# Performance work log

Measured on AMD Instinct MI355X. Metric: run time of the kernel, lower is better.

Reference implementation:

```python
import jax, jax.numpy as jnp
import numpy as np

B, C, H, W = 4, 64, 128, 128
HEADS, DIM_HEAD = 8, 64
INNER = HEADS * DIM_HEAD
EPS = 1e-12  # torch F.normalize default eps


def setup_inputs() -> dict:
    key = jax.random.key(0)
    ks = jax.random.split(key, 6)
    s_in = 1.0 / np.sqrt(C)
    s_pr = 1.0 / np.sqrt(INNER)
    return {
        "x_in": jax.random.normal(ks[0], (B, C, H, W), dtype=jnp.float32),
        "Wq": jax.random.uniform(ks[1], (C, INNER), jnp.float32, -s_in, s_in),
        "Wk": jax.random.uniform(ks[2], (C, INNER), jnp.float32, -s_in, s_in),
        "Wv": jax.random.uniform(ks[3], (C, INNER), jnp.float32, -s_in, s_in),
        "Wp": jax.random.uniform(ks[4], (INNER, C), jnp.float32, -s_pr, s_pr),
        "bp": jax.random.uniform(ks[5], (C,), jnp.float32, -s_pr, s_pr),
        "rescale": jnp.ones((HEADS, 1, 1), dtype=jnp.float32),
    }


def _l2norm(t):
    # normalize along last axis (the token axis n), matching F.normalize(p=2)
    n = jnp.sqrt(jnp.sum(t * t, axis=-1, keepdims=True))
    return t / jnp.maximum(n, EPS)


def reference(x_in, Wq, Wk, Wv, Wp, bp, rescale):
    b, c, h, w = x_in.shape
    n = h * w
    x = x_in.transpose(0, 2, 3, 1).reshape(b, n, c)  # [b, n, c]

    def heads_first(t):  # [b, n, inner] -> [b, heads, d, n]
        return t.reshape(b, n, HEADS, DIM_HEAD).transpose(0, 2, 3, 1)

    q = _l2norm(heads_first(x @ Wq))  # [b, H, d, n]
    k = _l2norm(heads_first(x @ Wk))
    v = heads_first(x @ Wv)

    # channel-channel attention: attn[d, e] = sum_n k[d, n] * q[e, n]
    attn = jnp.einsum('bhdn,bhen->bhde', k, q) * rescale  # [b, H, d, d]
    attn = jax.nn.softmax(attn, axis=-1)

    o = jnp.einsum('bhde,bhen->bhdn', attn, v)            # [b, H, d, n]
    o = o.transpose(0, 3, 1, 2).reshape(b, n, INNER)      # [b, n, inner]
    out = (o @ Wp + bp).reshape(b, h, w, c).transpose(0, 3, 1, 2)  # [b, c, h, w]
    return out, attn
```

## Files before the change

kernel.cpp:

```cpp
#include <hip/hip_runtime.h>
#include <math.h>

#define BB 4
#define CC 64
#define NN 16384
#define HEADS 8
#define INNER 512

__global__ __launch_bounds__(256) void k_gram(const float* __restrict__ x,
                                              float* __restrict__ part,
                                              int nslice) {
    const int s = blockIdx.x, b = blockIdx.y;
    const int t = threadIdx.x;
    const int g = t >> 6;
    const int lane = t & 63;
    const int ti = lane >> 3, tj = lane & 7;
    __shared__ float xs[64][65];
    float acc[8][8];
#pragma unroll
    for (int i = 0; i < 8; i++)
#pragma unroll
        for (int j = 0; j < 8; j++) acc[i][j] = 0.f;

    const float* xb = x + (size_t)b * CC * NN;
    const int cols = NN / nslice;
    const int ntiles = cols >> 6;
    const int nbase = s * cols;
    for (int tile = 0; tile < ntiles; ++tile) {
        const int n0 = nbase + tile * 64;
#pragma unroll
        for (int k = 0; k < 4; k++) {
            int f = k * 256 + t;
            int c = f >> 4, j4 = f & 15;
            const float4 v = *reinterpret_cast<const float4*>(xb + (size_t)c * NN + n0 + j4 * 4);
            xs[c][j4 * 4 + 0] = v.x; xs[c][j4 * 4 + 1] = v.y;
            xs[c][j4 * 4 + 2] = v.z; xs[c][j4 * 4 + 3] = v.w;
        }
        __syncthreads();
#pragma unroll
        for (int nn = 0; nn < 16; ++nn) {
            const int n = g * 16 + nn;
            float a[8], bv[8];
#pragma unroll
            for (int i = 0; i < 8; i++) a[i] = xs[ti * 8 + i][n];
#pragma unroll
            for (int j = 0; j < 8; j++) bv[j] = xs[tj * 8 + j][n];
#pragma unroll
            for (int i = 0; i < 8; i++)
#pragma unroll
                for (int j = 0; j < 8; j++)
                    acc[i][j] = fmaf(a[i], bv[j], acc[i][j]);
        }
        __syncthreads();
    }
    for (int gg = 0; gg < 4; ++gg) {
        if (g == gg) {
#pragma unroll
            for (int i = 0; i < 8; i++)
#pragma unroll
                for (int j = 0; j < 8; j++) {
                    if (gg == 0) xs[ti * 8 + i][tj * 8 + j] = acc[i][j];
                    else         xs[ti * 8 + i][tj * 8 + j] += acc[i][j];
                }
        }
        __syncthreads();
    }
    float* p = part + (size_t)(b * nslice + s) * 4096;
#pragma unroll
    for (int k = 0; k < 16; k++) {
        int f = k * 256 + t;
        p[f] = xs[f >> 6][f & 63];
    }
}

__global__ __launch_bounds__(256) void k_redG(const float* __restrict__ part,
                                              float* __restrict__ G,
                                              int nslice) {
    const int b = blockIdx.y;
    const int idx = blockIdx.x * 256 + threadIdx.x;
    const float* p = part + (size_t)b * nslice * 4096 + idx;
    float s0 = 0.f, s1 = 0.f, s2 = 0.f, s3 = 0.f;
    for (int s = 0; s < nslice; s += 4) {
        s0 += p[(size_t)s * 4096];
        s1 += p[(size_t)(s + 1) * 4096];
        s2 += p[(size_t)(s + 2) * 4096];
        s3 += p[(size_t)(s + 3) * 4096];
    }
    G[(size_t)b * 4096 + idx] = (s0 + s1) + (s2 + s3);
}

__global__ __launch_bounds__(256) void k_attn(const float* __restrict__ G,
                                              const float* __restrict__ Wq,
                                              const float* __restrict__ Wk,
                                              const float* __restrict__ Wv,
                                              const float* __restrict__ rescale,
                                              float* __restrict__ attn_out,
                                              float* __restrict__ wveff) {
    const int bh = blockIdx.x;
    const int b = bh >> 3, h = bh & 7;
    const int t = threadIdx.x;
    const int ti = t >> 4, tj = t & 15;
    __shared__ float Gs[64][65], Ws[64][65], Ts[64][65];
    __shared__ float qn[64], kn[64];

    for (int k = 0; k < 16; k++) { int f = k * 256 + t; Gs[f >> 6][f & 63] = G[(size_t)b * 4096 + f]; }
    for (int k = 0; k < 16; k++) { int f = k * 256 + t; int c = f >> 6, e = f & 63;
        Ws[c][e] = Wq[(size_t)c * INNER + h * 64 + e]; }
    __syncthreads();

    {
        float acc[4][4] = {};
        for (int c2 = 0; c2 < 64; c2++) {
            float a[4], bv[4];
#pragma unroll
            for (int i = 0; i < 4; i++) a[i] = Gs[ti * 4 + i][c2];
#pragma unroll
            for (int j = 0; j < 4; j++) bv[j] = Ws[c2][tj * 4 + j];
#pragma unroll
            for (int i = 0; i < 4; i++)
#pragma unroll
                for (int j = 0; j < 4; j++) acc[i][j] = fmaf(a[i], bv[j], acc[i][j]);
        }
#pragma unroll
        for (int i = 0; i < 4; i++)
#pragma unroll
            for (int j = 0; j < 4; j++) Ts[ti * 4 + i][tj * 4 + j] = acc[i][j];
    }
    __syncthreads();
    if (t < 64) {
        float s = 0.f;
        for (int c = 0; c < 64; c++) s += Ws[c][t] * Ts[c][t];
        qn[t] = fmaxf(sqrtf(s), 1e-12f);
    }
    __syncthreads();
    for (int k = 0; k < 16; k++) { int f = k * 256 + t; int c = f >> 6, e = f & 63;
        Ws[c][e] = Wk[(size_t)c * INNER + h * 64 + e]; }
    __syncthreads();

    float S[4][4] = {};
    for (int c = 0; c < 64; c++) {
        float a[4], bv[4];
#pragma unroll
        for (int i = 0; i < 4; i++) a[i] = Ws[c][ti * 4 + i];
#pragma unroll
        for (int j = 0; j < 4; j++) bv[j] = Ts[c][tj * 4 + j];
#pragma unroll
        for (int i = 0; i < 4; i++)
#pragma unroll
            for (int j = 0; j < 4; j++) S[i][j] = fmaf(a[i], bv[j], S[i][j]);
    }
    __syncthreads();

    {
        float acc[4][4] = {};
        for (int c2 = 0; c2 < 64; c2++) {
            float a[4], bv[4];
#pragma unroll
            for (int i = 0; i < 4; i++) a[i] = Gs[ti * 4 + i][c2];
#pragma unroll
            for (int j = 0; j < 4; j++) bv[j] = Ws[c2][tj * 4 + j];
#pragma unroll
            for (int i = 0; i < 4; i++)
#pragma unroll
                for (int j = 0; j < 4; j++) acc[i][j] = fmaf(a[i], bv[j], acc[i][j]);
        }
        __syncthreads();
#pragma unroll
        for (int i = 0; i < 4; i++)
#pragma unroll
            for (int j = 0; j < 4; j++) Ts[ti * 4 + i][tj * 4 + j] = acc[i][j];
    }
    __syncthreads();
    if (t < 64) {
        float s = 0.f;
        for (int c = 0; c < 64; c++) s += Ws[c][t] * Ts[c][t];
        kn[t] = fmaxf(sqrtf(s), 1e-12f);
    }
    __syncthreads();

    const float resc = rescale[h];
    float qinv[4];
#pragma unroll
    for (int j = 0; j < 4; j++) qinv[j] = 1.f / qn[tj * 4 + j];
    float p[4][4];
#pragma unroll
    for (int i = 0; i < 4; i++) {
        const float ki = resc / kn[ti * 4 + i];
        float m = -3.402823466e+38f;
#pragma unroll
        for (int j = 0; j < 4; j++) {
            float L = S[i][j] * ki * qinv[j];
            p[i][j] = L;
            m = fmaxf(m, L);
        }
        for (int o = 1; o < 16; o <<= 1) m = fmaxf(m, __shfl_xor(m, o, 64));
        float ssum = 0.f;
#pragma unroll
        for (int j = 0; j < 4; j++) { p[i][j] = expf(p[i][j] - m); ssum += p[i][j]; }
        for (int o = 1; o < 16; o <<= 1) ssum += __shfl_xor(ssum, o, 64);
        const float inv = 1.f / ssum;
#pragma unroll
        for (int j = 0; j < 4; j++) p[i][j] *= inv;
    }

    float* ao = attn_out + (size_t)bh * 64 * 64;
#pragma unroll
    for (int i = 0; i < 4; i++) {
        float4 v; v.x = p[i][0]; v.y = p[i][1]; v.z = p[i][2]; v.w = p[i][3];
        *reinterpret_cast<float4*>(ao + (size_t)(ti * 4 + i) * 64 + tj * 4) = v;
#pragma unroll
        for (int j = 0; j < 4; j++) Gs[ti * 4 + i][tj * 4 + j] = p[i][j];
    }
    __syncthreads();
    for (int k = 0; k < 16; k++) { int f = k * 256 + t; int c = f >> 6, e = f & 63;
        Ws[c][e] = Wv[(size_t)c * INNER + h * 64 + e]; }
    __syncthreads();

    {
        float acc[4][4] = {};
        for (int e = 0; e < 64; e++) {
            float a[4], bv[4];
#pragma unroll
            for (int i = 0; i < 4; i++) a[i] = Ws[ti * 4 + i][e];
#pragma unroll
            for (int j = 0; j < 4; j++) bv[j] = Gs[tj * 4 + j][e];
#pragma unroll
            for (int i = 0; i < 4; i++)
#pragma unroll
                for (int j = 0; j < 4; j++) acc[i][j] = fmaf(a[i], bv[j], acc[i][j]);
        }
        float* wvp = wveff + (size_t)b * CC * INNER;
#pragma unroll
        for (int i = 0; i < 4; i++) {
            float4 v; v.x = acc[i][0]; v.y = acc[i][1]; v.z = acc[i][2]; v.w = acc[i][3];
            *reinterpret_cast<float4*>(wvp + (size_t)(ti * 4 + i) * INNER + h * 64 + tj * 4) = v;
        }
    }
}

__global__ __launch_bounds__(256) void k_mpart(const float* __restrict__ wveff,
                                               const float* __restrict__ Wp,
                                               float* __restrict__ mpart) {
    const int cg = blockIdx.x, b = blockIdx.y;
    const int t = threadIdx.x, ti = t >> 4, tj = t & 15;
    __shared__ float Vs[64][65], Ps[64][65];
    float acc[4][4] = {};
    for (int sub = 0; sub < 2; ++sub) {
        const int hd0 = cg * 128 + sub * 64;
#pragma unroll
        for (int k = 0; k < 4; k++) {
            int f = k * 256 + t; int c = f >> 4, k4 = f & 15;
            float4 v = *reinterpret_cast<const float4*>(wveff + (size_t)b * CC * INNER + (size_t)c * INNER + hd0 + k4 * 4);
            Vs[c][k4 * 4 + 0] = v.x; Vs[c][k4 * 4 + 1] = v.y; Vs[c][k4 * 4 + 2] = v.z; Vs[c][k4 * 4 + 3] = v.w;
            float4 w = *reinterpret_cast<const float4*>(Wp + (size_t)(hd0 + c) * 64 + k4 * 4);
            Ps[c][k4 * 4 + 0] = w.x; Ps[c][k4 * 4 + 1] = w.y; Ps[c][k4 * 4 + 2] = w.z; Ps[c][k4 * 4 + 3] = w.w;
        }
        __syncthreads();
        for (int k = 0; k < 64; k++) {
            float a[4], bv[4];
#pragma unroll
            for (int i = 0; i < 4; i++) a[i] = Vs[ti * 4 + i][k];
#pragma unroll
            for (int j = 0; j < 4; j++) bv[j] = Ps[k][tj * 4 + j];
#pragma unroll
            for (int i = 0; i < 4; i++)
#pragma unroll
                for (int j = 0; j < 4; j++) acc[i][j] = fmaf(a[i], bv[j], acc[i][j]);
        }
        __syncthreads();
    }
    float* mp = mpart + (size_t)(b * 4 + cg) * 4096;
#pragma unroll
    for (int i = 0; i < 4; i++)
#pragma unroll
        for (int j = 0; j < 4; j++) mp[(ti * 4 + i) * 64 + tj * 4 + j] = acc[i][j];
}

__global__ __launch_bounds__(256) void k_out(const float* __restrict__ x,
                                             const float* __restrict__ mpart,
                                             const float* __restrict__ bp,
                                             float* __restrict__ out) {
    const int sn = blockIdx.x, b = blockIdx.y;
    const int t = threadIdx.x, ti = t >> 4, tj = t & 15;
    __shared__ float Ms[64][65], xs[64][65];
    const float* mp = mpart + (size_t)b * 4 * 4096;
#pragma unroll
    for (int k = 0; k < 16; k++) {
        int f = k * 256 + t;
        float s = mp[f] + mp[4096 + f] + mp[2 * 4096 + f] + mp[3 * 4096 + f];
        Ms[f >> 6][f & 63] = s;
    }
    const int n0 = sn * 64;
    const float* xb = x + (size_t)b * CC * NN;
#pragma unroll
    for (int k = 0; k < 4; k++) {
        int f = k * 256 + t; int c = f >> 4, j4 = f & 15;
        float4 v = *reinterpret_cast<const float4*>(xb + (size_t)c * NN + n0 + j4 * 4);
        xs[c][j4 * 4 + 0] = v.x; xs[c][j4 * 4 + 1] = v.y;
        xs[c][j4 * 4 + 2] = v.z; xs[c][j4 * 4 + 3] = v.w;
    }
    __syncthreads();
    float acc[4][4];
#pragma unroll
    for (int i = 0; i < 4; i++) {
        const float bv = bp[ti * 4 + i];
#pragma unroll
        for (int j = 0; j < 4; j++) acc[i][j] = bv;
    }
    for (int c = 0; c < 64; c++) {
        float m[4], xv[4];
#pragma unroll
        for (int i = 0; i < 4; i++) m[i] = Ms[c][ti * 4 + i];
#pragma unroll
        for (int j = 0; j < 4; j++) xv[j] = xs[c][tj * 4 + j];
#pragma unroll
        for (int i = 0; i < 4; i++)
#pragma unroll
            for (int j = 0; j < 4; j++) acc[i][j] = fmaf(m[i], xv[j], acc[i][j]);
    }
    float* ob = out + (size_t)b * CC * NN;
#pragma unroll
    for (int i = 0; i < 4; i++) {
        float4 v; v.x = acc[i][0]; v.y = acc[i][1]; v.z = acc[i][2]; v.w = acc[i][3];
        *reinterpret_cast<float4*>(ob + (size_t)(ti * 4 + i) * NN + n0 + tj * 4) = v;
    }
}

extern "C" void kernel_launch(void* const* d_in, const int* in_sizes, int n_in,
                              void* d_out, int out_size, void* d_ws, size_t ws_size,
                              hipStream_t stream) {
    const float* x  = (const float*)d_in[0];
    const float* Wq = (const float*)d_in[1];
    const float* Wk = (const float*)d_in[2];
    const float* Wv = (const float*)d_in[3];
    const float* Wp = (const float*)d_in[4];
    const float* bp = (const float*)d_in[5];
    const float* rescale = (const float*)d_in[6];
    float* out = (float*)d_out;
    float* attn_out = out + (size_t)BB * CC * NN;
    float* ws = (float*)d_ws;

    const size_t fixed_floats = (size_t)BB * 4096
                              + (size_t)BB * CC * INNER
                              + (size_t)BB * 4 * 4096;
    int nslice = 64;
    while (nslice > 4 &&
           ((size_t)BB * nslice * 4096 + fixed_floats) * sizeof(float) > ws_size)
        nslice >>= 1;

    float* part  = ws;
    float* G     = part + (size_t)BB * nslice * 4096;
    float* wveff = G + (size_t)BB * 4096;
    float* mpart = wveff + (size_t)BB * CC * INNER;

    hipLaunchKernelGGL(k_gram,  dim3(nslice, BB), dim3(256), 0, stream, x, part, nslice);
    hipLaunchKernelGGL(k_redG,  dim3(16, BB),     dim3(256), 0, stream, part, G, nslice);
    hipLaunchKernelGGL(k_attn,  dim3(BB * HEADS), dim3(256), 0, stream, G, Wq, Wk, Wv, rescale, attn_out, wveff);
    hipLaunchKernelGGL(k_mpart, dim3(4, BB),      dim3(256), 0, stream, wveff, Wp, mpart);
    hipLaunchKernelGGL(k_out,   dim3(NN / 64, BB), dim3(256), 0, stream, x, mpart, bp, out);
}
```

Measured before the change: 140.5 us.

## Fuse Wp projection into attention kernel with atomics and retile Gram kernel

Restructures the Gram kernel so each thread owns a 4x4 tile over the full 64-column tile with transposed float4 LDS reads, which removes the cross-wavegroup shared-memory reduction. The grid grows to 256 slices. The V-effective and Wp products are folded into k_attn, which atomically accumulates per-head contributions into a zeroed M buffer; this drops the k_mpart kernel and the wveff round trip through memory. Several kernels move to float4 LDS loads with padding of 68. In exchange it adds a memset, float atomics with nondeterministic summation order, and a larger partial buffer for k_redG to reduce.

```diff
diff --git a/kernel.cpp b/kernel.cpp
--- a/kernel.cpp
+++ b/kernel.cpp
@@ -12,15 +12,16 @@
                                               int nslice) {
     const int s = blockIdx.x, b = blockIdx.y;
     const int t = threadIdx.x;
-    const int g = t >> 6;
-    const int lane = t & 63;
-    const int ti = lane >> 3, tj = lane & 7;
-    __shared__ float xs[64][65];
-    float acc[8][8];
-#pragma unroll
-    for (int i = 0; i < 8; i++)
-#pragma unroll
-        for (int j = 0; j < 8; j++) acc[i][j] = 0.f;
+    const int g = t >> 6, lane = t & 63;
+    const int rg = lane >> 4;
+    const int r0 = g * 16 + rg * 4;
+    const int c0 = (lane & 15) * 4;
+    __shared__ float xs[64][68];
+    float acc[4][4];
+#pragma unroll
+    for (int i = 0; i < 4; i++)
+#pragma unroll
+        for (int j = 0; j < 4; j++) acc[i][j] = 0.f;
 
     const float* xb = x + (size_t)b * CC * NN;
     const int cols = NN / nslice;
@@ -33,43 +34,30 @@
             int f = k * 256 + t;
             int c = f >> 4, j4 = f & 15;
             const float4 v = *reinterpret_cast<const float4*>(xb + (size_t)c * NN + n0 + j4 * 4);
-            xs[c][j4 * 4 + 0] = v.x; xs[c][j4 * 4 + 1] = v.y;
-            xs[c][j4 * 4 + 2] = v.z; xs[c][j4 * 4 + 3] = v.w;
+            xs[j4 * 4 + 0][c] = v.x; xs[j4 * 4 + 1][c] = v.y;
+            xs[j4 * 4 + 2][c] = v.z; xs[j4 * 4 + 3][c] = v.w;
         }
         __syncthreads();
-#pragma unroll
-        for (int nn = 0; nn < 16; ++nn) {
-            const int n = g * 16 + nn;
-            float a[8], bv[8];
-#pragma unroll
-            for (int i = 0; i < 8; i++) a[i] = xs[ti * 8 + i][n];
-#pragma unroll
-            for (int j = 0; j < 8; j++) bv[j] = xs[tj * 8 + j][n];
-#pragma unroll
-            for (int i = 0; i < 8; i++)
-#pragma unroll
-                for (int j = 0; j < 8; j++)
-                    acc[i][j] = fmaf(a[i], bv[j], acc[i][j]);
+#pragma unroll 8
+        for (int n = 0; n < 64; ++n) {
+            const float4 a4 = *reinterpret_cast<const float4*>(&xs[n][r0]);
+            const float4 b4 = *reinterpret_cast<const float4*>(&xs[n][c0]);
+            acc[0][0] = fmaf(a4.x, b4.x, acc[0][0]); acc[0][1] = fmaf(a4.x, b4.y, acc[0][1]);
+            acc[0][2] = fmaf(a4.x, b4.z, acc[0][2]); acc[0][3] = fmaf(a4.x, b4.w, acc[0][3]);
+            acc[1][0] = fmaf(a4.y, b4.x, acc[1][0]); acc[1][1] = fmaf(a4.y, b4.y, acc[1][1]);
+            acc[1][2] = fmaf(a4.y, b4.z, acc[1][2]); acc[1][3] = fmaf(a4.y, b4.w, acc[1][3]);
+            acc[2][0] = fmaf(a4.z, b4.x, acc[2][0]); acc[2][1] = fmaf(a4.z, b4.y, acc[2][1]);
+            acc[2][2] = fmaf(a4.z, b4.z, acc[2][2]); acc[2][3] = fmaf(a4.z, b4.w, acc[2][3]);
+            acc[3][0] = fmaf(a4.w, b4.x, acc[3][0]); acc[3][1] = fmaf(a4.w, b4.y, acc[3][1]);
+            acc[3][2] = fmaf(a4.w, b4.z, acc[3][2]); acc[3][3] = fmaf(a4.w, b4.w, acc[3][3]);
         }
         __syncthreads();
     }
-    for (int gg = 0; gg < 4; ++gg) {
-        if (g == gg) {
-#pragma unroll
-            for (int i = 0; i < 8; i++)
-#pragma unroll
-                for (int j = 0; j < 8; j++) {
-                    if (gg == 0) xs[ti * 8 + i][tj * 8 + j] = acc[i][j];
-                    else         xs[ti * 8 + i][tj * 8 + j] += acc[i][j];
-                }
-        }
-        __syncthreads();
-    }
     float* p = part + (size_t)(b * nslice + s) * 4096;
 #pragma unroll
-    for (int k = 0; k < 16; k++) {
-        int f = k * 256 + t;
-        p[f] = xs[f >> 6][f & 63];
+    for (int i = 0; i < 4; i++) {
+        float4 v; v.x = acc[i][0]; v.y = acc[i][1]; v.z = acc[i][2]; v.w = acc[i][3];
+        *reinterpret_cast<float4*>(p + (r0 + i) * 64 + c0) = v;
     }
 }
 
@@ -93,14 +81,15 @@
                                               const float* __restrict__ Wq,
                                               const float* __restrict__ Wk,
                                               const float* __restrict__ Wv,
+                                              const float* __restrict__ Wp,
                                               const float* __restrict__ rescale,
                                               float* __restrict__ attn_out,
-                                              float* __restrict__ wveff) {
+                                              float* __restrict__ Mg) {
     const int bh = blockIdx.x;
     const int b = bh >> 3, h = bh & 7;
     const int t = threadIdx.x;
     const int ti = t >> 4, tj = t & 15;
-    __shared__ float Gs[64][65], Ws[64][65], Ts[64][65];
+    __shared__ float Gs[64][68], Ws[64][68], Ts[64][68];
     __shared__ float qn[64], kn[64];
 
     for (int k = 0; k < 16; k++) { int f = k * 256 + t; Gs[f >> 6][f & 63] = G[(size_t)b * 4096 + f]; }
@@ -110,12 +99,10 @@
 
     {
         float acc[4][4] = {};
-        for (int c2 = 0; c2 < 64; c2++) {
-            float a[4], bv[4];
-#pragma unroll
-            for (int i = 0; i < 4; i++) a[i] = Gs[ti * 4 + i][c2];
-#pragma unroll
-            for (int j = 0; j < 4; j++) bv[j] = Ws[c2][tj * 4 + j];
+        for (int k2 = 0; k2 < 64; k2++) {
+            const float4 a4 = *reinterpret_cast<const float4*>(&Gs[k2][ti * 4]);
+            const float4 b4 = *reinterpret_cast<const float4*>(&Ws[k2][tj * 4]);
+            float a[4] = {a4.x, a4.y, a4.z, a4.w}, bv[4] = {b4.x, b4.y, b4.z, b4.w};
 #pragma unroll
             for (int i = 0; i < 4; i++)
 #pragma unroll
@@ -138,27 +125,22 @@
     __syncthreads();
 
     float S[4][4] = {};
-    for (int c = 0; c < 64; c++) {
-        float a[4], bv[4];
-#pragma unroll
-        for (int i = 0; i < 4; i++) a[i] = Ws[c][ti * 4 + i];
-#pragma unroll
-        for (int j = 0; j < 4; j++) bv[j] = Ts[c][tj * 4 + j];
+    for (int k2 = 0; k2 < 64; k2++) {
+        const float4 a4 = *reinterpret_cast<const float4*>(&Ws[k2][ti * 4]);
+        const float4 b4 = *reinterpret_cast<const float4*>(&Ts[k2][tj * 4]);
+        float a[4] = {a4.x, a4.y, a4.z, a4.w}, bv[4] = {b4.x, b4.y, b4.z, b4.w};
 #pragma unroll
         for (int i = 0; i < 4; i++)
 #pragma unroll
             for (int j = 0; j < 4; j++) S[i][j] = fmaf(a[i], bv[j], S[i][j]);
     }
-    __syncthreads();
 
     {
         float acc[4][4] = {};
-        for (int c2 = 0; c2 < 64; c2++) {
-            float a[4], bv[4];
-#pragma unroll
-            for (int i = 0; i < 4; i++) a[i] = Gs[ti * 4 + i][c2];
-#pragma unroll
-            for (int j = 0; j < 4; j++) bv[j] = Ws[c2][tj * 4 + j];
+        for (int k2 = 0; k2 < 64; k2++) {
+            const float4 a4 = *reinterpret_cast<const float4*>(&Gs[k2][ti * 4]);
+            const float4 b4 = *reinterpret_cast<const float4*>(&Ws[k2][tj * 4]);
+            float a[4] = {a4.x, a4.y, a4.z, a4.w}, bv[4] = {b4.x, b4.y, b4.z, b4.w};
 #pragma unroll
             for (int i = 0; i < 4; i++)
 #pragma unroll
@@ -209,87 +191,57 @@
         float4 v; v.x = p[i][0]; v.y = p[i][1]; v.z = p[i][2]; v.w = p[i][3];
         *reinterpret_cast<float4*>(ao + (size_t)(ti * 4 + i) * 64 + tj * 4) = v;
 #pragma unroll
-        for (int j = 0; j < 4; j++) Gs[ti * 4 + i][tj * 4 + j] = p[i][j];
-    }
-    __syncthreads();
+        for (int j = 0; j < 4; j++) Ts[tj * 4 + j][ti * 4 + i] = p[i][j];
+    }
     for (int k = 0; k < 16; k++) { int f = k * 256 + t; int c = f >> 6, e = f & 63;
-        Ws[c][e] = Wv[(size_t)c * INNER + h * 64 + e]; }
-    __syncthreads();
-
-    {
-        float acc[4][4] = {};
-        for (int e = 0; e < 64; e++) {
-            float a[4], bv[4];
-#pragma unroll
-            for (int i = 0; i < 4; i++) a[i] = Ws[ti * 4 + i][e];
-#pragma unroll
-            for (int j = 0; j < 4; j++) bv[j] = Gs[tj * 4 + j][e];
-#pragma unroll
-            for (int i = 0; i < 4; i++)
-#pragma unroll
-                for (int j = 0; j < 4; j++) acc[i][j] = fmaf(a[i], bv[j], acc[i][j]);
-        }
-        float* wvp = wveff + (size_t)b * CC * INNER;
-#pragma unroll
-        for (int i = 0; i < 4; i++) {
-            float4 v; v.x = acc[i][0]; v.y = acc[i][1]; v.z = acc[i][2]; v.w = acc[i][3];
-            *reinterpret_cast<float4*>(wvp + (size_t)(ti * 4 + i) * INNER + h * 64 + tj * 4) = v;
-        }
-    }
-}
-
-__global__ __launch_bounds__(256) void k_mpart(const float* __restrict__ wveff,
-                                               const float* __restrict__ Wp,
-                                               float* __restrict__ mpart) {
-    const int cg = blockIdx.x, b = blockIdx.y;
-    const int t = threadIdx.x, ti = t >> 4, tj = t & 15;
-    __shared__ float Vs[64][65], Ps[64][65];
-    float acc[4][4] = {};
-    for (int sub = 0; sub < 2; ++sub) {
-        const int hd0 = cg * 128 + sub * 64;
-#pragma unroll
-        for (int k = 0; k < 4; k++) {
-            int f = k * 256 + t; int c = f >> 4, k4 = f & 15;
-            float4 v = *reinterpret_cast<const float4*>(wveff + (size_t)b * CC * INNER + (size_t)c * INNER + hd0 + k4 * 4);
-            Vs[c][k4 * 4 + 0] = v.x; Vs[c][k4 * 4 + 1] = v.y; Vs[c][k4 * 4 + 2] = v.z; Vs[c][k4 * 4 + 3] = v.w;
-            float4 w = *reinterpret_cast<const float4*>(Wp + (size_t)(hd0 + c) * 64 + k4 * 4);
-            Ps[c][k4 * 4 + 0] = w.x; Ps[c][k4 * 4 + 1] = w.y; Ps[c][k4 * 4 + 2] = w.z; Ps[c][k4 * 4 + 3] = w.w;
-        }
-        __syncthreads();
-        for (int k = 0; k < 64; k++) {
-            float a[4], bv[4];
-#pragma unroll
-            for (int i = 0; i < 4; i++) a[i] = Vs[ti * 4 + i][k];
-#pragma unroll
-            for (int j = 0; j < 4; j++) bv[j] = Ps[k][tj * 4 + j];
-#pragma unroll
-            for (int i = 0; i < 4; i++)
-#pragma unroll
-                for (int j = 0; j < 4; j++) acc[i][j] = fmaf(a[i], bv[j], acc[i][j]);
-        }
-        __syncthreads();
-    }
-    float* mp = mpart + (size_t)(b * 4 + cg) * 4096;
+        Ws[e][c] = Wv[(size_t)c * INNER + h * 64 + e]; }
+    __syncthreads();
+
+    float accv[4][4] = {};
+    for (int e = 0; e < 64; e++) {
+        const float4 a4 = *reinterpret_cast<const float4*>(&Ws[e][ti * 4]);
+        const float4 b4 = *reinterpret_cast<const float4*>(&Ts[e][tj * 4]);
+        float a[4] = {a4.x, a4.y, a4.z, a4.w}, bv[4] = {b4.x, b4.y, b4.z, b4.w};
+#pragma unroll
+        for (int i = 0; i < 4; i++)
+#pragma unroll
+            for (int j = 0; j < 4; j++) accv[i][j] = fmaf(a[i], bv[j], accv[i][j]);
+    }
+    __syncthreads();
 #pragma unroll
     for (int i = 0; i < 4; i++)
 #pragma unroll
-        for (int j = 0; j < 4; j++) mp[(ti * 4 + i) * 64 + tj * 4 + j] = acc[i][j];
+        for (int j = 0; j < 4; j++) Ts[tj * 4 + j][ti * 4 + i] = accv[i][j];
+    for (int k = 0; k < 16; k++) { int f = k * 256 + t;
+        Ws[f >> 6][f & 63] = Wp[(size_t)h * 4096 + f]; }
+    __syncthreads();
+
+    float accm[4][4] = {};
+    for (int d = 0; d < 64; d++) {
+        const float4 a4 = *reinterpret_cast<const float4*>(&Ts[d][ti * 4]);
+        const float4 b4 = *reinterpret_cast<const float4*>(&Ws[d][tj * 4]);
+        float a[4] = {a4.x, a4.y, a4.z, a4.w}, bv[4] = {b4.x, b4.y, b4.z, b4.w};
+#pragma unroll
+        for (int i = 0; i < 4; i++)
+#pragma unroll
+            for (int j = 0; j < 4; j++) accm[i][j] = fmaf(a[i], bv[j], accm[i][j]);
+    }
+    float* Mb = Mg + (size_t)b * 4096;
+#pragma unroll
+    for (int i = 0; i < 4; i++)
+#pragma unroll
+        for (int j = 0; j < 4; j++)
+            atomicAdd(&Mb[(ti * 4 + i) * 64 + tj * 4 + j], accm[i][j]);
 }
 
 __global__ __launch_bounds__(256) void k_out(const float* __restrict__ x,
-                                             const float* __restrict__ mpart,
+                                             const float* __restrict__ Mg,
                                              const float* __restrict__ bp,
                                              float* __restrict__ out) {
     const int sn = blockIdx.x, b = blockIdx.y;
     const int t = threadIdx.x, ti = t >> 4, tj = t & 15;
-    __shared__ float Ms[64][65], xs[64][65];
-    const float* mp = mpart + (size_t)b * 4 * 4096;
-#pragma unroll
-    for (int k = 0; k < 16; k++) {
-        int f = k * 256 + t;
-        float s = mp[f] + mp[4096 + f] + mp[2 * 4096 + f] + mp[3 * 4096 + f];
-        Ms[f >> 6][f & 63] = s;
-    }
+    __shared__ float Ms[64][68], xs[64][68];
+    for (int k = 0; k < 16; k++) { int f = k * 256 + t; Ms[f >> 6][f & 63] = Mg[(size_t)b * 4096 + f]; }
     const int n0 = sn * 64;
     const float* xb = x + (size_t)b * CC * NN;
 #pragma unroll
@@ -308,11 +260,9 @@
         for (int j = 0; j < 4; j++) acc[i][j] = bv;
     }
     for (int c = 0; c < 64; c++) {
-        float m[4], xv[4];
-#pragma unroll
-        for (int i = 0; i < 4; i++) m[i] = Ms[c][ti * 4 + i];
-#pragma unroll
-        for (int j = 0; j < 4; j++) xv[j] = xs[c][tj * 4 + j];
+        const float4 m4 = *reinterpret_cast<const float4*>(&Ms[c][ti * 4]);
+        const float4 x4 = *reinterpret_cast<const float4*>(&xs[c][tj * 4]);
+        float m[4] = {m4.x, m4.y, m4.z, m4.w}, xv[4] = {x4.x, x4.y, x4.z, x4.w};
 #pragma unroll
         for (int i = 0; i < 4; i++)
 #pragma unroll
@@ -341,21 +291,19 @@
     float* ws = (float*)d_ws;
 
     const size_t fixed_floats = (size_t)BB * 4096
-                              + (size_t)BB * CC * INNER
-                              + (size_t)BB * 4 * 4096;
-    int nslice = 64;
+                              + (size_t)BB * 4096;
+    int nslice = 256;
     while (nslice > 4 &&
            ((size_t)BB * nslice * 4096 + fixed_floats) * sizeof(float) > ws_size)
         nslice >>= 1;
 
-    float* part  = ws;
-    float* G     = part + (size_t)BB * nslice * 4096;
-    float* wveff = G + (size_t)BB * 4096;
-    float* mpart = wveff + (size_t)BB * CC * INNER;
-
-    hipLaunchKernelGGL(k_gram,  dim3(nslice, BB), dim3(256), 0, stream, x, part, nslice);
-    hipLaunchKernelGGL(k_redG,  dim3(16, BB),     dim3(256), 0, stream, part, G, nslice);
-    hipLaunchKernelGGL(k_attn,  dim3(BB * HEADS), dim3(256), 0, stream, G, Wq, Wk, Wv, rescale, attn_out, wveff);
-    hipLaunchKernelGGL(k_mpart, dim3(4, BB),      dim3(256), 0, stream, wveff, Wp, mpart);
-    hipLaunchKernelGGL(k_out,   dim3(NN / 64, BB), dim3(256), 0, stream, x, mpart, bp, out);
-}
+    float* part = ws;
+    float* G    = part + (size_t)BB * nslice * 4096;
+    float* Mg   = G + (size_t)BB * 4096;
+
+    hipMemsetAsync(Mg, 0, (size_t)BB * 4096 * sizeof(float), stream);
+    hipLaunchKernelGGL(k_gram,  dim3(nslice, BB),  dim3(256), 0, stream, x, part, nslice);
+    hipLaunchKernelGGL(k_redG,  dim3(16, BB),      dim3(256), 0, stream, part, G, nslice);
+    hipLaunchKernelGGL(k_attn,  dim3(BB * HEADS),  dim3(256), 0, stream, G, Wq, Wk, Wv, Wp, rescale, attn_out, Mg);
+    hipLaunchKernelGGL(k_out,   dim3(NN / 64, BB), dim3(256), 0, stream, x, Mg, bp, out);
+}
```

Result: faster. 137.6 us (-2.1%).
